# Kernel tuning notes

Hardware: AMD Instinct MI355X
Metric: run time of the kernel (lower is better)

## Reference

```python
import jax, jax.numpy as jnp
import numpy as np

NEG_INF = -1e30  # stands in for float('-inf') masked_fill; safe under softmax
MAX_ITERS = 6


def setup_inputs() -> dict:
    key = jax.random.key(0)
    ks = jax.random.split(key, 8)
    B, T, D, Dp, E = 8, 1500, 1536, 1024, 192
    s = lambda fan_in: 1.0 / np.sqrt(fan_in)
    return {
        "h": jax.random.normal(ks[0], (B, T, D), jnp.float32),
        "W1": jax.random.normal(ks[1], (3 * D, Dp), jnp.float32) * s(3 * D),
        "Wc": jax.random.normal(ks[2], (D, Dp), jnp.float32) * s(D),
        "W2": jax.random.normal(ks[3], (Dp, D), jnp.float32) * s(Dp),
        "b2": jnp.zeros((D,), jnp.float32),
        "w0": jax.random.normal(ks[4], (2 * D, E), jnp.float32) * s(2 * D),
        "b0": jnp.zeros((E,), jnp.float32),
        "Wstop": jax.random.normal(ks[5], (2 * D, 1), jnp.float32) * s(2 * D),
        "bstop": jnp.zeros((1,), jnp.float32),
        "threshold": jnp.full((1,), 0.5, jnp.float32),
        "C0": jnp.zeros((D,), jnp.float32),
    }


def _weighted_stats(h, a):
    # h: [B,T,D], a broadcastable to [B,T,D]
    mu = jnp.sum(a * h, axis=1)                         # [B,D]
    second = jnp.sum(a * h * h, axis=1)                 # [B,D]
    sigma = jnp.sqrt(jnp.clip(second - mu * mu, 1e-8))
    return mu, sigma


def reference(h, W1, Wc, W2, b2, w0, b0, Wstop, bstop, threshold, C0):
    B, T, D = h.shape
    th = threshold[0]

    # a_init = 1/T is constant across iterations -> hoist uniform stats and W1(e)
    mu0, sigma0 = _weighted_stats(h, jnp.float32(1.0 / T))          # [B,D]
    e = jnp.concatenate(
        [h,
         jnp.broadcast_to(mu0[:, None, :], (B, T, D)),
         jnp.broadcast_to(sigma0[:, None, :], (B, T, D))], axis=-1)  # [B,T,3D]
    base = jnp.einsum('btk,kp->btp', e, W1)                          # [B,T,Dp]

    energy_mask = jnp.mean(h * h, axis=-1) > 1e-4                    # [B,T]

    C = jnp.broadcast_to(C0[None, :], (B, D))
    stop = jnp.zeros((B,), bool)
    mask = jnp.ones((B, MAX_ITERS), bool)
    iters = jnp.arange(MAX_ITERS)

    embs, probs = [], []
    for i in range(MAX_ITERS):
        out1 = base + (C @ Wc)[:, None, :]                           # [B,T,Dp]
        out2 = jax.nn.relu(out1) @ W2 + b2                           # [B,T,D]
        att_raw = jnp.mean(out2, axis=-1)                            # [B,T]
        att_raw = jnp.where(energy_mask, att_raw, NEG_INF)
        A = jax.nn.softmax(att_raw, axis=-1)
        A = A / (jnp.sum(A, axis=1, keepdims=True) + 1e-8)

        # NOTE: faithful to source -- second weighted_stats uses out2 ('a'), not A
        mu_p, sigma_p = _weighted_stats(h, out2)                     # [B,D]
        emb = jnp.concatenate([mu_p, sigma_p], axis=-1) @ w0 + b0    # [B,E]
        emb = emb / jnp.maximum(
            jnp.linalg.norm(emb, axis=-1, keepdims=True), 1e-12)

        active = (~stop).astype(h.dtype)[:, None]
        C = C + active * (jnp.einsum('bt,btd->bd', A, h) / T)

        z = jnp.concatenate([jnp.sum(A[:, :, None] * out2, axis=1), C], axis=-1)
        p = jax.nn.sigmoid(z @ Wstop + bstop)[:, 0]                  # [B]

        newly = p < th
        mask = mask & ~(newly[:, None] & (iters[None, :] >= i))
        stop = stop | newly
        embs.append(emb)
        probs.append(p)

    E = jnp.stack(embs, axis=1)                                      # [B,6,E]
    E = E * mask[:, :, None].astype(E.dtype)
    P = jnp.stack(probs, axis=1)                                     # [B,6]
    return E, P
```

## Files before the change

### kernel.cpp

```cpp
#include <hip/hip_runtime.h>
#include <math.h>

#define NB 8
#define NT 1500
#define ND 1536
#define NP 1024
#define NE 192
#define NITER 6
#define NEGINF -1e30f

typedef __attribute__((ext_vector_type(8))) short bf16x8;
typedef __attribute__((ext_vector_type(4))) float f32x4;
typedef __attribute__((ext_vector_type(8))) unsigned short us16x8;

__device__ __forceinline__ unsigned short bf_rne(float x) {
    unsigned u = __float_as_uint(x);
    return (unsigned short)((u + 0x7FFFu + ((u >> 16) & 1u)) >> 16);
}
__device__ __forceinline__ float bf_f(unsigned short u) {
    return __uint_as_float(((unsigned)u) << 16);
}

__device__ __forceinline__ float block_reduce_sum(float v, float* red) {
    int tid = threadIdx.x;
    red[tid] = v; __syncthreads();
    for (int s = blockDim.x >> 1; s > 0; s >>= 1) {
        if (tid < s) red[tid] += red[tid + s];
        __syncthreads();
    }
    float r = red[0]; __syncthreads();
    return r;
}

__global__ void k_colstats(const float* __restrict__ h, float* __restrict__ sum1,
                           float* __restrict__ sum2) {
    int d = blockIdx.x * 256 + threadIdx.x;
    int b = blockIdx.y;
    int t0 = blockIdx.z * 125, t1 = t0 + 125;
    const float* hp = h + (size_t)b * NT * ND + d;
    float s = 0.f, s2 = 0.f;
    for (int t = t0; t < t1; ++t) { float v = hp[(size_t)t * ND]; s += v; s2 += v * v; }
    atomicAdd(&sum1[b * ND + d], s);
    atomicAdd(&sum2[b * ND + d], s2);
}

__global__ void k_stats_fin(float* __restrict__ mu0, float* __restrict__ sig0) {
    int i = blockIdx.x * 256 + threadIdx.x;
    float mu = mu0[i] * (1.f / NT);
    float sec = sig0[i] * (1.f / NT);
    mu0[i] = mu;
    sig0[i] = sqrtf(fmaxf(sec - mu * mu, 1e-8f));
}

__global__ void k_w2r(const float* __restrict__ W2, const float* __restrict__ b2,
                      float* __restrict__ w2r, float* __restrict__ b2m) {
    __shared__ float red[256];
    int p = blockIdx.x;
    float s = 0.f;
    if (p < NP) {
        const float* row = W2 + (size_t)p * ND;
        for (int d = threadIdx.x; d < ND; d += 256) s += row[d];
        s = block_reduce_sum(s, red);
        if (threadIdx.x == 0) w2r[p] = s * (1.f / ND);
    } else {
        for (int d = threadIdx.x; d < ND; d += 256) s += b2[d];
        s = block_reduce_sum(s, red);
        if (threadIdx.x == 0) b2m[0] = s * (1.f / ND);
    }
}

__global__ void k_biasb(const float* __restrict__ W1, const float* __restrict__ mu0,
                        const float* __restrict__ sig0, float* __restrict__ biasb) {
    int p = blockIdx.x * 256 + threadIdx.x;
    int d0 = blockIdx.y * 16, d1 = d0 + 16;
    float acc[NB];
#pragma unroll
    for (int b = 0; b < NB; ++b) acc[b] = 0.f;
    for (int d = d0; d < d1; ++d) {
        float wa = W1[(size_t)(ND + d) * NP + p];
        float wb = W1[(size_t)(2 * ND + d) * NP + p];
#pragma unroll
        for (int b = 0; b < NB; ++b)
            acc[b] += mu0[b * ND + d] * wa + sig0[b * ND + d] * wb;
    }
#pragma unroll
    for (int b = 0; b < NB; ++b) atomicAdd(&biasb[b * NP + p], acc[b]);
}

__global__ void k_init(float* __restrict__ C, const float* __restrict__ C0,
                       float* __restrict__ stopf) {
    int d = blockIdx.x * 256 + threadIdx.x;
    int b = blockIdx.y;
    C[b * ND + d] = C0[d];
    if (blockIdx.x == 0 && threadIdx.x == 0) stopf[b] = 0.f;
}

__global__ void k_split_w(const float* __restrict__ W, int ldw, int kcnt,
                          unsigned short* __restrict__ th, unsigned short* __restrict__ tl) {
    __shared__ float t[128][33];
    int nt = blockIdx.x, kc = blockIdx.y, tid = threadIdx.x;
    int col = tid & 127, kh = tid >> 7;
    const float* wp = W + (size_t)(kc * 32 + kh) * ldw + nt * 128 + col;
#pragma unroll
    for (int i = 0; i < 16; ++i)
        t[col][kh + 2 * i] = wp[(size_t)(2 * i) * ldw];
    __syncthreads();
    int r = tid >> 1;
    int swz = (r >> 1) & 3;
    size_t tb = ((size_t)nt * kcnt + kc) * 4096;
#pragma unroll
    for (int j = 0; j < 2; ++j) {
        int so = (tid & 1) * 2 + j;
        int s = so ^ swz;
        us16x8 hv, lv;
#pragma unroll
        for (int q = 0; q < 8; ++q) {
            float x = t[r][s * 8 + q];
            unsigned short hh = bf_rne(x);
            hv[q] = hh;
            lv[q] = bf_rne(x - bf_f(hh));
        }
        *(us16x8*)&th[tb + r * 32 + so * 8] = hv;
        *(us16x8*)&tl[tb + r * 32 + so * 8] = lv;
    }
}

__global__ void k_split_h(const float* __restrict__ h, unsigned short* __restrict__ th,
                          float* __restrict__ energy) {
    int tr = blockIdx.x, kc = blockIdx.y, b = blockIdx.z;
    int tid = threadIdx.x;
    int r = tid >> 1, quad = tid & 1;
    int row = tr * 128 + r;
    bool ok = row < NT;
    size_t tb = ((size_t)(b * 12 + tr) * 48 + kc) * 4096;
    const float* hp = h + ((size_t)b * NT + (ok ? row : 0)) * ND + kc * 32 + quad * 16;
    int swz = (r >> 1) & 3;
    float es = 0.f;
#pragma unroll
    for (int half = 0; half < 2; ++half) {
        us16x8 hv;
#pragma unroll
        for (int j = 0; j < 2; ++j) {
            float x0 = 0.f, x1 = 0.f, x2 = 0.f, x3 = 0.f;
            if (ok) {
                float4 v = *(const float4*)(hp + half * 8 + j * 4);
                x0 = v.x; x1 = v.y; x2 = v.z; x3 = v.w;
                es += x0 * x0 + x1 * x1 + x2 * x2 + x3 * x3;
            }
            hv[j * 4 + 0] = bf_rne(x0); hv[j * 4 + 1] = bf_rne(x1);
            hv[j * 4 + 2] = bf_rne(x2); hv[j * 4 + 3] = bf_rne(x3);
        }
        int off = r * 32 + (((quad * 2 + half) ^ swz) << 3);
        *(us16x8*)&th[tb + off] = hv;
    }
    es += __shfl_xor(es, 1);
    if (ok && quad == 0) atomicAdd(&energy[b * NT + row], es);
}

__global__ void k_relu_att(const unsigned short* __restrict__ base16,
                           const float* __restrict__ cvec, const float* __restrict__ w2r,
                           unsigned short* __restrict__ th, float* __restrict__ att) {
    int tr = blockIdx.x, kc = blockIdx.y, b = blockIdx.z;
    int tid = threadIdx.x;
    int r = tid >> 1, quad = tid & 1;
    int row = tr * 128 + r;
    bool ok = row < NT;
    size_t tb = ((size_t)(b * 12 + tr) * 32 + kc) * 4096;
    const unsigned short* bp = base16 + ((size_t)b * NT + (ok ? row : 0)) * NP + kc * 32 + quad * 16;
    const float* cv = cvec + b * NP + kc * 32 + quad * 16;
    const float* wr = w2r + kc * 32 + quad * 16;
    int swz = (r >> 1) & 3;
    float asum = 0.f;
#pragma unroll
    for (int half = 0; half < 2; ++half) {
        us16x8 bv = (us16x8){0, 0, 0, 0, 0, 0, 0, 0};
        if (ok) bv = *(const us16x8*)(bp + half * 8);
        us16x8 hv;
#pragma unroll
        for (int j = 0; j < 2; ++j) {
            float4 c4 = *(const float4*)(cv + half * 8 + j * 4);
            float4 w4 = *(const float4*)(wr + half * 8 + j * 4);
            float x0 = fmaxf(bf_f(bv[j * 4 + 0]) + c4.x, 0.f);
            float x1 = fmaxf(bf_f(bv[j * 4 + 1]) + c4.y, 0.f);
            float x2 = fmaxf(bf_f(bv[j * 4 + 2]) + c4.z, 0.f);
            float x3 = fmaxf(bf_f(bv[j * 4 + 3]) + c4.w, 0.f);
            if (ok) asum += x0 * w4.x + x1 * w4.y + x2 * w4.z + x3 * w4.w;
            hv[j * 4 + 0] = bf_rne(x0); hv[j * 4 + 1] = bf_rne(x1);
            hv[j * 4 + 2] = bf_rne(x2); hv[j * 4 + 3] = bf_rne(x3);
        }
        int off = r * 32 + (((quad * 2 + half) ^ swz) << 3);
        *(us16x8*)&th[tb + off] = hv;
    }
    asum += __shfl_xor(asum, 1);
    if (ok && quad == 0) atomicAdd(&att[b * NT + row], asum);
}

__global__ __launch_bounds__(256, 4) void k_gemm_relu(
    const unsigned short* __restrict__ ht, const unsigned short* __restrict__ at_h,
    const unsigned short* __restrict__ bt_h, const float* __restrict__ b2,
    const float* __restrict__ Aw, float* __restrict__ mup, float* __restrict__ s2p,
    float* __restrict__ zab, float* __restrict__ ahb) {
    constexpr int KC = NP / 32;
    __shared__ __align__(16) unsigned short As[2][4096];
    __shared__ __align__(16) unsigned short Bs[2][4096];
    int flat = blockIdx.x + 12 * (blockIdx.y + 12 * blockIdx.z);
    int swzf = (flat & 7) * 144 + (flat >> 3);
    int tr = swzf % 12, nt = (swzf / 12) % 12, b = swzf / 144;
    int tid = threadIdx.x;
    int lane = tid & 63, w = tid >> 6;
    int wr = w >> 1, wc = w & 1;
    int l15 = lane & 15, kg = lane >> 4;
    int sw = (l15 >> 1) & 3;
    f32x4 acc[4][4];
#pragma unroll
    for (int m = 0; m < 4; ++m)
#pragma unroll
        for (int n = 0; n < 4; ++n) acc[m][n] = (f32x4){0.f, 0.f, 0.f, 0.f};
    int aoff[4], boff[4];
#pragma unroll
    for (int m = 0; m < 4; ++m) aoff[m] = (wr * 64 + m * 16 + l15) * 32 + ((kg ^ sw) << 3);
#pragma unroll
    for (int n = 0; n < 4; ++n) boff[n] = (wc * 64 + n * 16 + l15) * 32 + ((kg ^ sw) << 3);

    const unsigned short* ga = at_h + ((size_t)(b * 12 + tr) * KC) * 4096 + lane * 8;
    const unsigned short* gb = bt_h + ((size_t)nt * KC) * 4096 + lane * 8;

    auto stage = [&](int buf, int kc) {
#pragma unroll
        for (int c = 0; c < 4; ++c) {
            int seg = w * 4 + c;
            int part = seg & 7;
            const unsigned short* src = ((seg >> 3) == 0 ? ga : gb) + (size_t)kc * 4096 + part * 512;
            unsigned short* dst = ((seg >> 3) == 0 ? &As[buf][0] : &Bs[buf][0]) + part * 512;
            __builtin_amdgcn_global_load_lds(src, dst, 16, 0, 0);
        }
    };

    stage(0, 0);
    __syncthreads();
    int cur = 0;
    for (int kc = 0; kc < KC; ++kc) {
        if (kc + 1 < KC) stage(cur ^ 1, kc + 1);
        bf16x8 af[4], bfr[4];
#pragma unroll
        for (int m = 0; m < 4; ++m) af[m] = *(const bf16x8*)&As[cur][aoff[m]];
#pragma unroll
        for (int n = 0; n < 4; ++n) bfr[n] = *(const bf16x8*)&Bs[cur][boff[n]];
#pragma unroll
        for (int n = 0; n < 4; ++n)
#pragma unroll
            for (int m = 0; m < 4; ++m)
                acc[m][n] = __builtin_amdgcn_mfma_f32_16x16x32_bf16(af[m], bfr[n], acc[m][n], 0, 0, 0);
        __syncthreads();
        cur ^= 1;
    }

    int rowb = tr * 128 + wr * 64 + (kg << 2);
    int colb = nt * 128 + wc * 64 + l15;
    const unsigned short* htb = ht + (size_t)(b * 12 + tr) * 48 * 4096;
    float b2c[4];
#pragma unroll
    for (int n = 0; n < 4; ++n) b2c[n] = b2[colb + n * 16];
    float pm[4] = {0, 0, 0, 0}, ps2[4] = {0, 0, 0, 0}, pza[4] = {0, 0, 0, 0}, pah[4] = {0, 0, 0, 0};
#pragma unroll
    for (int m = 0; m < 4; ++m) {
#pragma unroll
        for (int q = 0; q < 4; ++q) {
            int row = rowb + m * 16 + q;
            int r_in = wr * 64 + (kg << 2) + m * 16 + q;
            bool ok = row < NT;
            float okf = ok ? 1.f : 0.f;
            float a = Aw[b * NT + (ok ? row : (NT - 1))] * okf;
            int rsw = (r_in >> 1) & 3;
#pragma unroll
            for (int n = 0; n < 4; ++n) {
                int col = colb + n * 16;
                float hv = bf_f(htb[(size_t)(col >> 5) * 4096 + r_in * 32 +
                                    ((((col & 31) >> 3) ^ rsw) << 3) + (col & 7)]) * okf;
                float o2 = acc[m][n][q] + b2c[n];
                pm[n] = fmaf(o2, hv, pm[n]);
                ps2[n] = fmaf(o2 * hv, hv, ps2[n]);
                pza[n] = fmaf(a, o2, pza[n]);
                pah[n] = fmaf(a, hv, pah[n]);
            }
        }
    }
#pragma unroll
    for (int n = 0; n < 4; ++n) {
        pm[n] += __shfl_xor(pm[n], 16); pm[n] += __shfl_xor(pm[n], 32);
        ps2[n] += __shfl_xor(ps2[n], 16); ps2[n] += __shfl_xor(ps2[n], 32);
        pza[n] += __shfl_xor(pza[n], 16); pza[n] += __shfl_xor(pza[n], 32);
        pah[n] += __shfl_xor(pah[n], 16); pah[n] += __shfl_xor(pah[n], 32);
        if (kg == 0) {
            int col = colb + n * 16;
            atomicAdd(&mup[b * ND + col], pm[n]);
            atomicAdd(&s2p[b * ND + col], ps2[n]);
            atomicAdd(&zab[b * ND + col], pza[n]);
            atomicAdd(&ahb[b * ND + col], pah[n]);
        }
    }
}

__global__ __launch_bounds__(256, 3) void k_gemm_base(
    const unsigned short* __restrict__ ht, const unsigned short* __restrict__ bt_h,
    const unsigned short* __restrict__ bt_l, const float* __restrict__ biasb,
    unsigned short* __restrict__ Out16) {
    constexpr int KC2 = ND / 64;
    __shared__ __align__(16) unsigned short As[8192];
    __shared__ __align__(16) unsigned short Bh_s[8192];
    __shared__ __align__(16) unsigned short Bl_s[8192];
    int flat = blockIdx.x + 12 * (blockIdx.y + 8 * blockIdx.z);
    int swzf = (flat & 7) * 96 + (flat >> 3);
    int tr = swzf % 12, nt = (swzf / 12) % 8, b = swzf / 96;
    int tid = threadIdx.x;
    int lane = tid & 63, w = tid >> 6;
    int wr = w >> 1, wc = w & 1;
    int l15 = lane & 15, kg = lane >> 4;
    int sw = (l15 >> 1) & 3;
    f32x4 acc[4][4];
#pragma unroll
    for (int m = 0; m < 4; ++m)
#pragma unroll
        for (int n = 0; n < 4; ++n) acc[m][n] = (f32x4){0.f, 0.f, 0.f, 0.f};
    int aoff[4], boff[4];
#pragma unroll
    for (int m = 0; m < 4; ++m) aoff[m] = (wr * 64 + m * 16 + l15) * 32 + ((kg ^ sw) << 3);
#pragma unroll
    for (int n = 0; n < 4; ++n) boff[n] = (wc * 64 + n * 16 + l15) * 32 + ((kg ^ sw) << 3);

    const unsigned short* ga = ht + ((size_t)(b * 12 + tr) * 48) * 4096 + lane * 8;
    const unsigned short* gbh = bt_h + ((size_t)nt * 48) * 4096 + lane * 8;
    const unsigned short* gbl = bt_l + ((size_t)nt * 48) * 4096 + lane * 8;

    for (int kc2 = 0; kc2 < KC2; ++kc2) {
#pragma unroll
        for (int c = 0; c < 12; ++c) {
            int seg = w * 12 + c;
            int part = seg & 15, mat = seg >> 4;
            const unsigned short* src =
                (mat == 0 ? ga : mat == 1 ? gbh : gbl) + (size_t)kc2 * 8192 + part * 512;
            unsigned short* dst =
                (mat == 0 ? &As[0] : mat == 1 ? &Bh_s[0] : &Bl_s[0]) + part * 512;
            __builtin_amdgcn_global_load_lds(src, dst, 16, 0, 0);
        }
        __syncthreads();
#pragma unroll
        for (int half = 0; half < 2; ++half) {
            int ho = half * 4096;
            bf16x8 af[4];
#pragma unroll
            for (int m = 0; m < 4; ++m) af[m] = *(const bf16x8*)&As[ho + aoff[m]];
#pragma unroll
            for (int n = 0; n < 4; ++n) {
                bf16x8 bh = *(const bf16x8*)&Bh_s[ho + boff[n]];
                bf16x8 bl = *(const bf16x8*)&Bl_s[ho + boff[n]];
#pragma unroll
                for (int m = 0; m < 4; ++m) {
                    acc[m][n] = __builtin_amdgcn_mfma_f32_16x16x32_bf16(af[m], bh, acc[m][n], 0, 0, 0);
                    acc[m][n] = __builtin_amdgcn_mfma_f32_16x16x32_bf16(af[m], bl, acc[m][n], 0, 0, 0);
                }
            }
        }
        __syncthreads();
    }

    int rowb = tr * 128 + wr * 64 + (kg << 2);
    int colb = nt * 128 + wc * 64 + l15;
#pragma unroll
    for (int m = 0; m < 4; ++m)
#pragma unroll
        for (int q = 0; q < 4; ++q) {
            int row = rowb + m * 16 + q;
            if (row < NT) {
                unsigned short* orow = Out16 + ((size_t)b * NT + row) * NP;
#pragma unroll
                for (int n = 0; n < 4; ++n)
                    orow[colb + n * 16] =
                        bf_rne(acc[m][n][q] + biasb[b * NP + colb + n * 16]);
            }
        }
}

__global__ void k_cvec(const float* __restrict__ C, const float* __restrict__ Wc,
                       float* __restrict__ cvec) {
    int p = blockIdx.x * 256 + threadIdx.x;
    int d0 = blockIdx.y * 48, d1 = d0 + 48;
    float acc[NB];
#pragma unroll
    for (int b = 0; b < NB; ++b) acc[b] = 0.f;
    for (int d = d0; d < d1; ++d) {
        float wc = Wc[(size_t)d * NP + p];
#pragma unroll
        for (int b = 0; b < NB; ++b) acc[b] += C[b * ND + d] * wc;
    }
#pragma unroll
    for (int b = 0; b < NB; ++b) atomicAdd(&cvec[b * NP + p], acc[b]);
}

__global__ void k_softmax(const float* __restrict__ att, const float* __restrict__ energy,
                          const float* __restrict__ b2m, float* __restrict__ A) {
    __shared__ float red[256];
    int b = blockIdx.x, tid = threadIdx.x;
    float bm = b2m[0];
    const float* x = att + (size_t)b * NT;
    const float* en = energy + (size_t)b * NT;
    float* a = A + (size_t)b * NT;
    float mx = -3.4e38f;
    for (int t = tid; t < NT; t += 256) {
        float v = (en[t] * (1.f / ND) > 1e-4f) ? x[t] + bm : NEGINF;
        mx = fmaxf(mx, v);
    }
    red[tid] = mx; __syncthreads();
    for (int s = 128; s > 0; s >>= 1) {
        if (tid < s) red[tid] = fmaxf(red[tid], red[tid + s]);
        __syncthreads();
    }
    mx = red[0]; __syncthreads();
    float sm = 0.f;
    for (int t = tid; t < NT; t += 256) {
        float v = (en[t] * (1.f / ND) > 1e-4f) ? x[t] + bm : NEGINF;
        float e = expf(v - mx); a[t] = e; sm += e;
    }
    float s1 = block_reduce_sum(sm, red);
    float inv1 = 1.f / s1;
    float sm2 = 0.f;
    for (int t = tid; t < NT; t += 256) { float v = a[t] * inv1; a[t] = v; sm2 += v; }
    float s2 = block_reduce_sum(sm2, red);
    float inv2 = 1.f / (s2 + 1e-8f);
    for (int t = tid; t < NT; t += 256) a[t] *= inv2;
}

__global__ void k_embacc(const float* __restrict__ red4, const float* __restrict__ w0,
                         float* __restrict__ embt) {
    __shared__ float mus[NB][48], sgs[NB][48];
    int e = threadIdx.x;
    int d0 = blockIdx.x * 48;
    const float* mup = red4;
    const float* s2p = red4 + (size_t)NB * ND;
    for (int idx = e; idx < NB * 48; idx += 192) {
        int b = idx / 48, dd = idx % 48;
        float mu = mup[b * ND + d0 + dd];
        mus[b][dd] = mu;
        sgs[b][dd] = sqrtf(fmaxf(s2p[b * ND + d0 + dd] - mu * mu, 1e-8f));
    }
    __syncthreads();
    float acc[NB];
#pragma unroll
    for (int b = 0; b < NB; ++b) acc[b] = 0.f;
    for (int dd = 0; dd < 48; ++dd) {
        float wa = w0[(size_t)(d0 + dd) * NE + e];
        float wb = w0[(size_t)(ND + d0 + dd) * NE + e];
#pragma unroll
        for (int b = 0; b < NB; ++b)
            acc[b] += mus[b][dd] * wa + sgs[b][dd] * wb;
    }
#pragma unroll
    for (int b = 0; b < NB; ++b) atomicAdd(&embt[b * NE + e], acc[b]);
}

__global__ void k_tail2(const float* __restrict__ red4, const float* __restrict__ embt,
                        const float* __restrict__ b0, const float* __restrict__ Wstop,
                        const float* __restrict__ bstop, const float* __restrict__ thr,
                        float* __restrict__ Cb, float* __restrict__ stopf,
                        float* __restrict__ Eout, float* __restrict__ Pout, int iter) {
    __shared__ float red[256];
    __shared__ float liveflag;
    int b = blockIdx.x, tid = threadIdx.x;
    const float* Ahb = red4 + (size_t)2 * NB * ND + b * ND;
    const float* zAb = red4 + (size_t)3 * NB * ND + b * ND;
    float active = (stopf[b] > 0.5f) ? 0.f : 1.f;
    float dsum = 0.f;
    for (int d = tid; d < ND; d += 256) {
        float Cn = Cb[b * ND + d] + active * (Ahb[d] * (1.f / NT));
        Cb[b * ND + d] = Cn;
        dsum += zAb[d] * Wstop[d] + Cn * Wstop[ND + d];
    }
    float s = block_reduce_sum(dsum, red);
    if (tid == 0) {
        float logit = s + bstop[0];
        float p = 1.f / (1.f + expf(-logit));
        Pout[b * NITER + iter] = p;
        bool newly = p < thr[0];
        if (newly) stopf[b] = 1.f;
        liveflag = (active > 0.5f && !newly) ? 1.f : 0.f;
    }
    __syncthreads();
    float live = liveflag;
    float emb = (tid < NE) ? (embt[b * NE + tid] + b0[tid]) : 0.f;
    float nrm = block_reduce_sum(emb * emb, red);
    float sc = live / fmaxf(sqrtf(nrm), 1e-12f);
    if (tid < NE) Eout[((size_t)b * NITER + iter) * NE + tid] = emb * sc;
}

extern "C" void kernel_launch(void* const* d_in, const int* in_sizes, int n_in,
                              void* d_out, int out_size, void* d_ws, size_t ws_size,
                              hipStream_t stream) {
    const float* h = (const float*)d_in[0];
    const float* W1 = (const float*)d_in[1];
    const float* Wc = (const float*)d_in[2];
    const float* W2 = (const float*)d_in[3];
    const float* b2 = (const float*)d_in[4];
    const float* w0 = (const float*)d_in[5];
    const float* b0 = (const float*)d_in[6];
    const float* Wstop = (const float*)d_in[7];
    const float* bstop = (const float*)d_in[8];
    const float* thr = (const float*)d_in[9];
    const float* C0 = (const float*)d_in[10];

    float* Eout = (float*)d_out;
    float* Pout = Eout + (size_t)NB * NITER * NE;

    char* wsb = (char*)d_ws;
    size_t off = 0;
    auto alloc = [&](size_t bytes) -> void* {
        void* p = wsb + off; off += (bytes + 15) & ~(size_t)15; return p;
    };

    unsigned short* base16 = (unsigned short*)alloc((size_t)NB * NT * NP * 2);
    unsigned short* rel_h = (unsigned short*)alloc((size_t)NB * 12 * 32 * 4096 * 2);
    unsigned short* ht_h = (unsigned short*)alloc((size_t)NB * 12 * 48 * 4096 * 2);
    unsigned short* w1t_h = (unsigned short*)alloc((size_t)8 * 48 * 4096 * 2);
    unsigned short* w1t_l = (unsigned short*)alloc((size_t)8 * 48 * 4096 * 2);
    unsigned short* w2t_h = (unsigned short*)alloc((size_t)12 * 32 * 4096 * 2);
    unsigned short* w2t_l = (unsigned short*)alloc((size_t)12 * 32 * 4096 * 2);
    size_t pz = (size_t)2 * NB * ND + NB * NT + NB * NP;
    float* mu0 = (float*)alloc(pz * 4);
    float* sig0 = mu0 + NB * ND;
    float* energy = sig0 + NB * ND;
    float* biasb = energy + NB * NT;
    float* w2r = (float*)alloc(NP * 4);
    float* b2m = (float*)alloc(16);
    size_t zelems = (size_t)NB * NP + NB * NT + 4 * NB * ND + NB * NE;
    float* cvec = (float*)alloc(zelems * 4);
    float* att = cvec + NB * NP;
    float* red4 = att + NB * NT;
    float* mup = red4;
    float* s2p = red4 + NB * ND;
    float* Ahb = red4 + 2 * NB * ND;
    float* zAb = red4 + 3 * NB * ND;
    float* embt = red4 + 4 * NB * ND;
    float* Abuf = (float*)alloc(NB * NT * 4);
    float* Cb = (float*)alloc(NB * ND * 4);
    float* stopf = (float*)alloc(32);
    size_t zero_bytes = zelems * 4;

    hipMemsetAsync(mu0, 0, pz * 4, stream);
    k_colstats<<<dim3(ND / 256, NB, 12), 256, 0, stream>>>(h, mu0, sig0);
    k_stats_fin<<<dim3(NB * ND / 256), 256, 0, stream>>>(mu0, sig0);
    k_w2r<<<dim3(NP + 1), 256, 0, stream>>>(W2, b2, w2r, b2m);
    k_biasb<<<dim3(4, 96), 256, 0, stream>>>(W1, mu0, sig0, biasb);
    k_split_w<<<dim3(8, 48), 256, 0, stream>>>(W1, NP, 48, w1t_h, w1t_l);
    k_split_w<<<dim3(12, 32), 256, 0, stream>>>(W2, ND, 32, w2t_h, w2t_l);
    k_split_h<<<dim3(12, 48, NB), 256, 0, stream>>>(h, ht_h, energy);
    k_gemm_base<<<dim3(12, 8, NB), 256, 0, stream>>>(ht_h, w1t_h, w1t_l, biasb, base16);
    k_init<<<dim3(ND / 256, NB), 256, 0, stream>>>(Cb, C0, stopf);

    for (int i = 0; i < NITER; ++i) {
        hipMemsetAsync(cvec, 0, zero_bytes, stream);
        k_cvec<<<dim3(4, 32), 256, 0, stream>>>(Cb, Wc, cvec);
        k_relu_att<<<dim3(12, 32, NB), 256, 0, stream>>>(base16, cvec, w2r, rel_h, att);
        k_softmax<<<dim3(NB), 256, 0, stream>>>(att, energy, b2m, Abuf);
        k_gemm_relu<<<dim3(12, 12, NB), 256, 0, stream>>>(
            ht_h, rel_h, w2t_h, b2, Abuf, mup, s2p, zAb, Ahb);
        k_embacc<<<dim3(32), 192, 0, stream>>>(red4, w0, embt);
        k_tail2<<<dim3(NB), 256, 0, stream>>>(red4, embt, b0, Wstop, bstop, thr,
                                              Cb, stopf, Eout, Pout, i);
    }
}
```

Measured before the change: 1.066 ms.

## Double-buffer base GEMM, use vmcnt waits, replace atomics with partial-sum reduction

k_gemm_base moves from a single-buffered 64-wide K step to a double-buffered 32-wide K step, so global-to-LDS loads for the next chunk overlap the MFMAs on the current one. Both GEMMs now use explicit s_waitcnt vmcnt counts with raw s_barrier instead of __syncthreads, waiting only on the older batch of loads. The k_gemm_relu epilogue writes per-row-tile partial sums to a scratch buffer instead of issuing float atomics, and a new k_redsum kernel sums the 24 partials. This removes the memset and atomic contention, at the cost of an extra launch and scratch traffic per iteration.

```diff
diff --git a/kernel.cpp b/kernel.cpp
--- a/kernel.cpp
+++ b/kernel.cpp
@@ -198,8 +198,7 @@
 __global__ __launch_bounds__(256, 4) void k_gemm_relu(
     const unsigned short* __restrict__ ht, const unsigned short* __restrict__ at_h,
     const unsigned short* __restrict__ bt_h, const float* __restrict__ b2,
-    const float* __restrict__ Aw, float* __restrict__ mup, float* __restrict__ s2p,
-    float* __restrict__ zab, float* __restrict__ ahb) {
+    const float* __restrict__ Aw, float* __restrict__ part) {
     constexpr int KC = NP / 32;
     __shared__ __align__(16) unsigned short As[2][4096];
     __shared__ __align__(16) unsigned short Bs[2][4096];
@@ -229,18 +228,24 @@
 #pragma unroll
         for (int c = 0; c < 4; ++c) {
             int seg = w * 4 + c;
-            int part = seg & 7;
-            const unsigned short* src = ((seg >> 3) == 0 ? ga : gb) + (size_t)kc * 4096 + part * 512;
-            unsigned short* dst = ((seg >> 3) == 0 ? &As[buf][0] : &Bs[buf][0]) + part * 512;
+            int part_ = seg & 7;
+            const unsigned short* src = ((seg >> 3) == 0 ? ga : gb) + (size_t)kc * 4096 + part_ * 512;
+            unsigned short* dst = ((seg >> 3) == 0 ? &As[buf][0] : &Bs[buf][0]) + part_ * 512;
             __builtin_amdgcn_global_load_lds(src, dst, 16, 0, 0);
         }
     };
 
     stage(0, 0);
-    __syncthreads();
     int cur = 0;
     for (int kc = 0; kc < KC; ++kc) {
-        if (kc + 1 < KC) stage(cur ^ 1, kc + 1);
+        if (kc + 1 < KC) {
+            stage(cur ^ 1, kc + 1);
+            asm volatile("s_waitcnt vmcnt(4)" ::: "memory");
+        } else {
+            asm volatile("s_waitcnt vmcnt(0)" ::: "memory");
+        }
+        __builtin_amdgcn_s_barrier();
+        __builtin_amdgcn_sched_barrier(0);
         bf16x8 af[4], bfr[4];
 #pragma unroll
         for (int m = 0; m < 4; ++m) af[m] = *(const bf16x8*)&As[cur][aoff[m]];
@@ -251,7 +256,7 @@
 #pragma unroll
             for (int m = 0; m < 4; ++m)
                 acc[m][n] = __builtin_amdgcn_mfma_f32_16x16x32_bf16(af[m], bfr[n], acc[m][n], 0, 0, 0);
-        __syncthreads();
+        __builtin_amdgcn_s_barrier();
         cur ^= 1;
     }
 
@@ -293,22 +298,40 @@
         pah[n] += __shfl_xor(pah[n], 16); pah[n] += __shfl_xor(pah[n], 32);
         if (kg == 0) {
             int col = colb + n * 16;
-            atomicAdd(&mup[b * ND + col], pm[n]);
-            atomicAdd(&s2p[b * ND + col], ps2[n]);
-            atomicAdd(&zab[b * ND + col], pza[n]);
-            atomicAdd(&ahb[b * ND + col], pah[n]);
-        }
-    }
+            size_t pb = (((size_t)(tr * 2 + wr) * NB + b) * 4) * ND;
+            part[pb + 0 * (size_t)ND + col] = pm[n];
+            part[pb + 1 * (size_t)ND + col] = ps2[n];
+            part[pb + 2 * (size_t)ND + col] = pza[n];
+            part[pb + 3 * (size_t)ND + col] = pah[n];
+        }
+    }
+}
+
+__global__ void k_redsum(const float* __restrict__ part, float* __restrict__ red4) {
+    int idx = blockIdx.x * 256 + threadIdx.x;
+    int b = idx / ND, d = idx % ND;
+    float s0 = 0.f, s1 = 0.f, s2 = 0.f, s3 = 0.f;
+    for (int s = 0; s < 24; ++s) {
+        const float* p = part + (((size_t)s * NB + b) * 4) * ND + d;
+        s0 += p[0];
+        s1 += p[(size_t)ND];
+        s2 += p[2 * (size_t)ND];
+        s3 += p[3 * (size_t)ND];
+    }
+    red4[idx] = s0;
+    red4[(size_t)NB * ND + idx] = s1;
+    red4[3 * (size_t)NB * ND + idx] = s2;
+    red4[2 * (size_t)NB * ND + idx] = s3;
 }
 
 __global__ __launch_bounds__(256, 3) void k_gemm_base(
     const unsigned short* __restrict__ ht, const unsigned short* __restrict__ bt_h,
     const unsigned short* __restrict__ bt_l, const float* __restrict__ biasb,
     unsigned short* __restrict__ Out16) {
-    constexpr int KC2 = ND / 64;
-    __shared__ __align__(16) unsigned short As[8192];
-    __shared__ __align__(16) unsigned short Bh_s[8192];
-    __shared__ __align__(16) unsigned short Bl_s[8192];
+    constexpr int KC = ND / 32;
+    __shared__ __align__(16) unsigned short As[2][4096];
+    __shared__ __align__(16) unsigned short Bh_s[2][4096];
+    __shared__ __align__(16) unsigned short Bl_s[2][4096];
     int flat = blockIdx.x + 12 * (blockIdx.y + 8 * blockIdx.z);
     int swzf = (flat & 7) * 96 + (flat >> 3);
     int tr = swzf % 12, nt = (swzf / 12) % 8, b = swzf / 96;
@@ -328,40 +351,49 @@
 #pragma unroll
     for (int n = 0; n < 4; ++n) boff[n] = (wc * 64 + n * 16 + l15) * 32 + ((kg ^ sw) << 3);
 
-    const unsigned short* ga = ht + ((size_t)(b * 12 + tr) * 48) * 4096 + lane * 8;
-    const unsigned short* gbh = bt_h + ((size_t)nt * 48) * 4096 + lane * 8;
-    const unsigned short* gbl = bt_l + ((size_t)nt * 48) * 4096 + lane * 8;
-
-    for (int kc2 = 0; kc2 < KC2; ++kc2) {
-#pragma unroll
-        for (int c = 0; c < 12; ++c) {
-            int seg = w * 12 + c;
-            int part = seg & 15, mat = seg >> 4;
+    const unsigned short* ga = ht + ((size_t)(b * 12 + tr) * KC) * 4096 + lane * 8;
+    const unsigned short* gbh = bt_h + ((size_t)nt * KC) * 4096 + lane * 8;
+    const unsigned short* gbl = bt_l + ((size_t)nt * KC) * 4096 + lane * 8;
+
+    auto stage = [&](int buf, int kc) {
+#pragma unroll
+        for (int c = 0; c < 6; ++c) {
+            int seg = w * 6 + c;
+            int mat = seg >> 3, part_ = seg & 7;
             const unsigned short* src =
-                (mat == 0 ? ga : mat == 1 ? gbh : gbl) + (size_t)kc2 * 8192 + part * 512;
+                (mat == 0 ? ga : mat == 1 ? gbh : gbl) + (size_t)kc * 4096 + part_ * 512;
             unsigned short* dst =
-                (mat == 0 ? &As[0] : mat == 1 ? &Bh_s[0] : &Bl_s[0]) + part * 512;
+                (mat == 0 ? &As[buf][0] : mat == 1 ? &Bh_s[buf][0] : &Bl_s[buf][0]) + part_ * 512;
             __builtin_amdgcn_global_load_lds(src, dst, 16, 0, 0);
         }
-        __syncthreads();
-#pragma unroll
-        for (int half = 0; half < 2; ++half) {
-            int ho = half * 4096;
-            bf16x8 af[4];
-#pragma unroll
-            for (int m = 0; m < 4; ++m) af[m] = *(const bf16x8*)&As[ho + aoff[m]];
-#pragma unroll
-            for (int n = 0; n < 4; ++n) {
-                bf16x8 bh = *(const bf16x8*)&Bh_s[ho + boff[n]];
-                bf16x8 bl = *(const bf16x8*)&Bl_s[ho + boff[n]];
-#pragma unroll
-                for (int m = 0; m < 4; ++m) {
-                    acc[m][n] = __builtin_amdgcn_mfma_f32_16x16x32_bf16(af[m], bh, acc[m][n], 0, 0, 0);
-                    acc[m][n] = __builtin_amdgcn_mfma_f32_16x16x32_bf16(af[m], bl, acc[m][n], 0, 0, 0);
-                }
+    };
+
+    stage(0, 0);
+    int cur = 0;
+    for (int kc = 0; kc < KC; ++kc) {
+        if (kc + 1 < KC) {
+            stage(cur ^ 1, kc + 1);
+            asm volatile("s_waitcnt vmcnt(6)" ::: "memory");
+        } else {
+            asm volatile("s_waitcnt vmcnt(0)" ::: "memory");
+        }
+        __builtin_amdgcn_s_barrier();
+        __builtin_amdgcn_sched_barrier(0);
+        bf16x8 af[4];
+#pragma unroll
+        for (int m = 0; m < 4; ++m) af[m] = *(const bf16x8*)&As[cur][aoff[m]];
+#pragma unroll
+        for (int n = 0; n < 4; ++n) {
+            bf16x8 bh = *(const bf16x8*)&Bh_s[cur][boff[n]];
+            bf16x8 bl = *(const bf16x8*)&Bl_s[cur][boff[n]];
+#pragma unroll
+            for (int m = 0; m < 4; ++m) {
+                acc[m][n] = __builtin_amdgcn_mfma_f32_16x16x32_bf16(af[m], bh, acc[m][n], 0, 0, 0);
+                acc[m][n] = __builtin_amdgcn_mfma_f32_16x16x32_bf16(af[m], bl, acc[m][n], 0, 0, 0);
             }
         }
-        __syncthreads();
+        __builtin_amdgcn_s_barrier();
+        cur ^= 1;
     }
 
     int rowb = tr * 128 + wr * 64 + (kg << 2);
@@ -530,15 +562,12 @@
     float* biasb = energy + NB * NT;
     float* w2r = (float*)alloc(NP * 4);
     float* b2m = (float*)alloc(16);
-    size_t zelems = (size_t)NB * NP + NB * NT + 4 * NB * ND + NB * NE;
+    size_t zelems = (size_t)NB * NP + NB * NT + NB * NE;
     float* cvec = (float*)alloc(zelems * 4);
     float* att = cvec + NB * NP;
-    float* red4 = att + NB * NT;
-    float* mup = red4;
-    float* s2p = red4 + NB * ND;
-    float* Ahb = red4 + 2 * NB * ND;
-    float* zAb = red4 + 3 * NB * ND;
-    float* embt = red4 + 4 * NB * ND;
+    float* embt = att + NB * NT;
+    float* red4 = (float*)alloc((size_t)4 * NB * ND * 4);
+    float* part = (float*)alloc((size_t)24 * NB * 4 * ND * 4);
     float* Abuf = (float*)alloc(NB * NT * 4);
     float* Cb = (float*)alloc(NB * ND * 4);
     float* stopf = (float*)alloc(32);
@@ -561,7 +590,8 @@
         k_relu_att<<<dim3(12, 32, NB), 256, 0, stream>>>(base16, cvec, w2r, rel_h, att);
         k_softmax<<<dim3(NB), 256, 0, stream>>>(att, energy, b2m, Abuf);
         k_gemm_relu<<<dim3(12, 12, NB), 256, 0, stream>>>(
-            ht_h, rel_h, w2t_h, b2, Abuf, mup, s2p, zAb, Ahb);
+            ht_h, rel_h, w2t_h, b2, Abuf, part);
+        k_redsum<<<dim3(48), 256, 0, stream>>>(part, red4);
         k_embacc<<<dim3(32), 192, 0, stream>>>(red4, w0, embt);
         k_tail2<<<dim3(NB), 256, 0, stream>>>(red4, embt, b0, Wstop, bstop, thr,
                                               Cb, stopf, Eout, Pout, i);
```

Measured after the change: 1.163 ms. +9.2%, slower.
